# Optimization experiments

Hardware: AMD Instinct MI355X
Metric: run time of the kernel (lower is better)

The kernel has to match this reference:

```python
import jax, jax.numpy as jnp
import numpy as np

V, H, O = 256, 1024, 1024   # input_dim, hidden_dim, output_dim
B, T = 64, 512


def setup_inputs() -> dict:
    key = jax.random.key(0)
    ks = jax.random.split(key, 12)
    s = 1.0 / np.sqrt(H)  # torch nn.RNN / nn.Linear init range
    u = lambda k, shp: jax.random.uniform(k, shp, jnp.float32, -s, s)
    return {
        "x": jax.random.randint(ks[0], (B, T), 0, V),
        "W_ih_f": u(ks[1], (H, V)), "W_hh_f": u(ks[2], (H, H)),
        "b_ih_f": u(ks[3], (H,)),   "b_hh_f": u(ks[4], (H,)),
        "W_ih_b": u(ks[5], (H, V)), "W_hh_b": u(ks[6], (H, H)),
        "b_ih_b": u(ks[7], (H,)),   "b_hh_b": u(ks[8], (H,)),
        "W_fc": u(ks[9], (O, 2 * H)), "b_fc": u(ks[10], (O,)),
    }


def _scan_rnn(xW, W_hh):
    # xW: [T,B,H] precomputed input contribution (x W_ih^T + b_ih + b_hh)
    def step(h, xw):
        h = jnp.tanh(xw + h @ W_hh.T)
        return h, h
    h0 = jnp.zeros((xW.shape[1], W_hh.shape[0]), xW.dtype)
    _, hs = jax.lax.scan(step, h0, xW)
    return hs  # [T,B,H]


def reference(x, W_ih_f, W_hh_f, b_ih_f, b_hh_f,
              W_ih_b, W_hh_b, b_ih_b, b_hh_b, W_fc, b_fc):
    # one_hot(x, V) @ W_ih^T  ==  W_ih.T[x]  (gather; same math, no dense one-hot)
    xW_f = W_ih_f.T[x] + b_ih_f + b_hh_f          # [B,T,H]
    xW_b = W_ih_b.T[x] + b_ih_b + b_hh_b          # [B,T,H]
    hf = _scan_rnn(jnp.swapaxes(xW_f, 0, 1), W_hh_f)            # [T,B,H]
    hb = _scan_rnn(jnp.swapaxes(xW_b, 0, 1)[::-1], W_hh_b)[::-1]  # [T,B,H]
    out = jnp.swapaxes(jnp.concatenate([hf, hb], axis=-1), 0, 1)  # [B,T,2H]
    return out @ W_fc.T + b_fc                    # [B,T,O]
```

## Files before the change

### kernel.cpp

```cpp
#include <hip/hip_runtime.h>
#include <math.h>

#define B_ 64
#define T_ 512
#define H_ 1024
#define V_ 256
#define O_ 1024
#define KFC 2048

typedef short bf16x8 __attribute__((ext_vector_type(8)));
typedef _Float16 f16x8 __attribute__((ext_vector_type(8)));
typedef float f32x4 __attribute__((ext_vector_type(4)));
typedef int   i32x4 __attribute__((ext_vector_type(4)));
typedef unsigned long long u64x2 __attribute__((ext_vector_type(2)));

#define FLIP64 0x8000800080008000ULL

#define OFF_TABLE_F 0
#define OFF_TABLE_B 1048576
#define OFF_XT      2097152
#define OFF_WHH     2228224
#define OFF_WFC     6422528
#define OFF_HSF     10616832
#define OFF_HSB     77725696

__global__ void prep_kernel(const int* __restrict__ x,
    const float* __restrict__ WihF, const float* __restrict__ WhhF,
    const float* __restrict__ bihF, const float* __restrict__ bhhF,
    const float* __restrict__ WihB, const float* __restrict__ WhhB,
    const float* __restrict__ bihB, const float* __restrict__ bhhB,
    const float* __restrict__ Wfc,
    float* __restrict__ tableF, float* __restrict__ tableB,
    int* __restrict__ xT, short* __restrict__ whhpack,
    short* __restrict__ wfcpack, unsigned long long* __restrict__ hsz)
{
  const long NT1 = 524288, NT2 = 32768, NT3 = 2097152, NT4 = 2097152;
  const long NT5 = 16777216;
  const long total = NT1 + NT2 + NT3 + NT4 + NT5;
  for (long i = (long)blockIdx.x * blockDim.x + threadIdx.x; i < total;
       i += (long)gridDim.x * blockDim.x) {
    long j = i;
    if (j < NT1) {
      int d = (int)(j >> 18);
      int r = (int)(j & 262143);
      int v = r >> 10, h = r & 1023;
      const float* Wih = d ? WihB : WihF;
      const float* bi  = d ? bihB : bihF;
      const float* bh  = d ? bhhB : bhhF;
      (d ? tableB : tableF)[r] = Wih[h * V_ + v] + bi[h] + bh[h];
      continue;
    }
    j -= NT1;
    if (j < NT2) {
      int t = (int)(j >> 6), bb = (int)(j & 63);
      xT[j] = x[bb * T_ + t];
      continue;
    }
    j -= NT2;
    if (j < NT3) {
      int d = (int)(j >> 20);
      int r = (int)(j & 1048575);
      int jj = r & 7;
      int lanei = (r >> 3) & 63;
      int kt = (r >> 9) & 31;
      int cti = (r >> 14) & 3;
      int csi = (r >> 16) & 15;
      int c = csi * 64 + cti * 16 + (lanei & 15);
      int k = kt * 32 + (lanei >> 4) * 8 + jj;
      float w = (d ? WhhB : WhhF)[c * H_ + k];
      _Float16 wh = (_Float16)w;
      whhpack[j] = __builtin_bit_cast(short, wh);
      continue;
    }
    j -= NT3;
    if (j < NT4) {
      int jj = (int)(j & 7);
      int lanei = (int)((j >> 3) & 63);
      int nti = (int)((j >> 9) & 3);
      int k32 = (int)((j >> 11) & 63);
      int obi = (int)(j >> 17);
      int o = obi * 64 + nti * 16 + (lanei & 15);
      int k = k32 * 32 + (lanei >> 4) * 8 + jj;
      _Float16 wf = (_Float16)Wfc[(long)o * KFC + k];
      wfcpack[j] = __builtin_bit_cast(short, wf);
      continue;
    }
    j -= NT4;
    hsz[j] = 0ULL;
    continue;
  }
}

__global__ __launch_bounds__(256, 1)
void rnn_kernel(const int* __restrict__ xT,
                const float* __restrict__ tableF, const float* __restrict__ tableB,
                const short* __restrict__ whhpack,
                unsigned long long* __restrict__ hsfF,
                unsigned long long* __restrict__ hsfB)
{
  extern __shared__ char lds[];
  char* ldsW = lds;
  char* ldsH = lds + 131072;
  const int tid = threadIdx.x;
  const int wg = blockIdx.x;
  const int dir = wg >> 6;
  const int bt = (wg >> 4) & 3;
  const int cs = wg & 15;
  const int lane = tid & 63;
  const int ct = tid >> 6;
  const int row = bt * 16 + (lane & 15);
  const int c4 = cs * 64 + ct * 16 + (lane >> 4) * 4;
  const float* table = dir ? tableB : tableF;
  unsigned long long* hsx = dir ? hsfB : hsfF;
  const int pub_off = bt * 4096 + (c4 >> 5) * 128 + ((c4 >> 2) & 1) * 64 +
                      (lane & 15) + ((c4 >> 3) & 3) * 16;

  {
    const i32x4* wsrc = (const i32x4*)whhpack + (size_t)(dir * 16 + cs) * 8192;
    i32x4* wdst = (i32x4*)ldsW;
    #pragma unroll
    for (int it = 0; it < 32; ++it)
      wdst[it * 256 + tid] = wsrc[it * 256 + tid];
  }
  __syncthreads();

  const f32x4 zv = {0.f, 0.f, 0.f, 0.f};

  {
    int t0 = dir ? 511 : 0;
    int v = xT[t0 * 64 + row];
    f32x4 xwv = *(const f32x4*)(table + v * 1024 + c4);
    unsigned long long hx = 0;
    #pragma unroll
    for (int r = 0; r < 4; ++r) {
      float e = __expf(2.0f * xwv[r]);
      float h = (e - 1.0f) / (e + 1.0f);
      union { _Float16 f; unsigned short u; } cv; cv.f = (_Float16)h;
      unsigned short u = (cv.u == 0x8000u) ? 0u : cv.u;
      hx |= (unsigned long long)(u ^ 0x8000u) << (16 * r);
    }
    __hip_atomic_store(hsx + (size_t)t0 * 16384 + pub_off, hx,
                       __ATOMIC_RELAXED, __HIP_MEMORY_SCOPE_AGENT);
  }

  for (int s = 1; s < 512; ++s) {
    const int t = dir ? (511 - s) : s;
    const int tprev = dir ? (t + 1) : (t - 1);
    int v = xT[t * 64 + row];
    f32x4 xwv = *(const f32x4*)(table + v * 1024 + c4);

    const unsigned long long* sp =
        hsx + (size_t)tprev * 16384 + bt * 4096 + tid * 2;
    unsigned long long va[8], vb[8];
    for (;;) {
      int miss = 0;
      #pragma unroll
      for (int jj = 0; jj < 8; ++jj) {
        va[jj] = __hip_atomic_load(sp + jj * 512, __ATOMIC_RELAXED,
                                   __HIP_MEMORY_SCOPE_AGENT);
        vb[jj] = __hip_atomic_load(sp + jj * 512 + 1, __ATOMIC_RELAXED,
                                   __HIP_MEMORY_SCOPE_AGENT);
      }
      #pragma unroll
      for (int jj = 0; jj < 8; ++jj)
        miss |= (va[jj] == 0ULL) | (vb[jj] == 0ULL);
      if (!__ballot(miss)) break;
      __builtin_amdgcn_s_sleep(1);
    }
    #pragma unroll
    for (int jj = 0; jj < 8; ++jj) {
      u64x2 w; w[0] = va[jj] ^ FLIP64; w[1] = vb[jj] ^ FLIP64;
      *(u64x2*)(ldsH + jj * 4096 + tid * 16) = w;
    }
    __syncthreads();

    f32x4 acc4[4] = {zv, zv, zv, zv};
    #pragma unroll
    for (int kt = 0; kt < 32; ++kt) {
      f16x8 af = *(const f16x8*)(ldsW + ((ct * 32 + kt) * 64 + lane) * 16);
      u64x2 bv;
      bv[0] = *(const unsigned long long*)(ldsH + (kt * 128 + lane) * 8);
      bv[1] = *(const unsigned long long*)(ldsH + (kt * 128 + 64 + lane) * 8);
      f16x8 bf = __builtin_bit_cast(f16x8, bv);
      acc4[kt & 3] =
          __builtin_amdgcn_mfma_f32_16x16x32_f16(af, bf, acc4[kt & 3], 0, 0, 0);
    }
    __syncthreads();

    f32x4 accs = (acc4[0] + acc4[1]) + (acc4[2] + acc4[3]);
    unsigned long long hx = 0;
    #pragma unroll
    for (int r = 0; r < 4; ++r) {
      float zz = accs[r] + xwv[r];
      float e = __expf(2.0f * zz);
      float h = (e - 1.0f) / (e + 1.0f);
      union { _Float16 f; unsigned short u; } cv; cv.f = (_Float16)h;
      unsigned short u = (cv.u == 0x8000u) ? 0u : cv.u;
      hx |= (unsigned long long)(u ^ 0x8000u) << (16 * r);
    }
    __hip_atomic_store(hsx + (size_t)t * 16384 + pub_off, hx,
                       __ATOMIC_RELAXED, __HIP_MEMORY_SCOPE_AGENT);
  }
}

__global__ __launch_bounds__(256, 4)
void fc_kernel(const unsigned long long* __restrict__ hsfF,
               const unsigned long long* __restrict__ hsfB,
               const short* __restrict__ wfcpack, const float* __restrict__ bfc,
               float* __restrict__ out)
{
  __shared__ unsigned long long Alds[1024];
  __shared__ short Blds[4096];
  const int tid = threadIdx.x;
  const int lane = tid & 63;
  const int wv = tid >> 6;
  const int mt2 = wv & 1;
  const int nt2 = wv >> 1;
  const int t = blockIdx.x;
  const int ob = blockIdx.y;
  const int ik = tid >> 7;
  const int btl = (tid >> 5) & 3;
  const int w4 = (tid & 31) * 4;

  const i32x4 flip32 = {(int)0x80008000, (int)0x80008000,
                        (int)0x80008000, (int)0x80008000};
  f32x4 z = {0.f, 0.f, 0.f, 0.f};
  f32x4 acc[2][2] = {{z, z}, {z, z}};

  for (int kc = 0; kc < 32; ++kc) {
    {
      const unsigned long long* src =
          (kc < 16 ? hsfF : hsfB) + (size_t)t * 16384;
      int kt0 = (kc & 15) * 2;
      const unsigned long long* ap = src + btl * 4096 + (kt0 + ik) * 128 + w4;
      i32x4 a01 = *(const i32x4*)ap ^ flip32;
      i32x4 a23 = *(const i32x4*)(ap + 2) ^ flip32;
      *(i32x4*)&Alds[(btl * 2 + ik) * 128 + w4] = a01;
      *(i32x4*)&Alds[(btl * 2 + ik) * 128 + w4 + 2] = a23;
    }
    {
      const i32x4* src = (const i32x4*)(wfcpack + ((size_t)ob * 64 + kc * 2) * 2048);
      i32x4* dst = (i32x4*)Blds;
      dst[tid] = src[tid];
      dst[tid + 256] = src[tid + 256];
    }
    __syncthreads();
    #pragma unroll
    for (int k2 = 0; k2 < 2; ++k2) {
      f16x8 afr[2];
      #pragma unroll
      for (int mi = 0; mi < 2; ++mi) {
        int btm = mt2 * 2 + mi;
        u64x2 av;
        av[0] = Alds[(btm * 2 + k2) * 128 + lane];
        av[1] = Alds[(btm * 2 + k2) * 128 + 64 + lane];
        afr[mi] = __builtin_bit_cast(f16x8, av);
      }
      #pragma unroll
      for (int ni = 0; ni < 2; ++ni) {
        int ntg = nt2 * 2 + ni;
        f16x8 bfr = *(const f16x8*)((const char*)Blds + ((k2 * 4 + ntg) * 64 + lane) * 16);
        #pragma unroll
        for (int mi = 0; mi < 2; ++mi)
          acc[mi][ni] = __builtin_amdgcn_mfma_f32_16x16x32_f16(afr[mi], bfr, acc[mi][ni], 0, 0, 0);
      }
    }
    __syncthreads();
  }
  #pragma unroll
  for (int mi = 0; mi < 2; ++mi) {
    #pragma unroll
    for (int ni = 0; ni < 2; ++ni) {
      int o = ob * 64 + nt2 * 32 + ni * 16 + (lane & 15);
      float bias = bfc[o];
      #pragma unroll
      for (int r = 0; r < 4; ++r) {
        int b = mt2 * 32 + mi * 16 + (lane >> 4) * 4 + r;
        out[(size_t)(b * 512 + t) * O_ + o] = acc[mi][ni][r] + bias;
      }
    }
  }
}

extern "C" void kernel_launch(void* const* d_in, const int* in_sizes, int n_in,
                              void* d_out, int out_size, void* d_ws, size_t ws_size,
                              hipStream_t stream) {
  const int* x = (const int*)d_in[0];
  const float* WihF = (const float*)d_in[1];
  const float* WhhF = (const float*)d_in[2];
  const float* bihF = (const float*)d_in[3];
  const float* bhhF = (const float*)d_in[4];
  const float* WihB = (const float*)d_in[5];
  const float* WhhB = (const float*)d_in[6];
  const float* bihB = (const float*)d_in[7];
  const float* bhhB = (const float*)d_in[8];
  const float* Wfc  = (const float*)d_in[9];
  const float* bfc  = (const float*)d_in[10];
  float* out = (float*)d_out;
  char* ws = (char*)d_ws;

  float* tableF = (float*)(ws + OFF_TABLE_F);
  float* tableB = (float*)(ws + OFF_TABLE_B);
  int* xT = (int*)(ws + OFF_XT);
  short* whhpack = (short*)(ws + OFF_WHH);
  short* wfcpack = (short*)(ws + OFF_WFC);
  unsigned long long* hsfF = (unsigned long long*)(ws + OFF_HSF);
  unsigned long long* hsfB = (unsigned long long*)(ws + OFF_HSB);

  hipFuncSetAttribute((const void*)rnn_kernel,
                      hipFuncAttributeMaxDynamicSharedMemorySize, 163840);

  prep_kernel<<<dim3(2048), dim3(256), 0, stream>>>(
      x, WihF, WhhF, bihF, bhhF, WihB, WhhB, bihB, bhhB, Wfc,
      tableF, tableB, xT, whhpack, wfcpack, hsfF);
  rnn_kernel<<<dim3(128), dim3(256), 163840, stream>>>(
      xT, tableF, tableB, whhpack, hsfF, hsfB);
  fc_kernel<<<dim3(512, 16), dim3(256), 0, stream>>>(
      hsfF, hsfB, wfcpack, bfc, out);
}
```

Measured before the change: 1.583 ms.

## Feed recurrent MFMAs directly from global hidden state with pipelined polling

Each wave now loads its own B-operand fragments of the previous hidden state straight from global memory into registers, in four K-groups. It polls each group for readiness and overlaps issuing the next group's loads with MFMAs on the current group. This removes the LDS staging buffer and both per-step __syncthreads barriers, so the dynamic LDS request drops. The cost is that every wave issues its own redundant global loads and spin-waits, which adds memory traffic and register pressure.

```diff
diff --git a/kernel.cpp b/kernel.cpp
--- a/kernel.cpp
+++ b/kernel.cpp
@@ -100,7 +100,6 @@
 {
   extern __shared__ char lds[];
   char* ldsW = lds;
-  char* ldsH = lds + 131072;
   const int tid = threadIdx.x;
   const int wg = blockIdx.x;
   const int dir = wg >> 6;
@@ -150,42 +149,61 @@
     f32x4 xwv = *(const f32x4*)(table + v * 1024 + c4);
 
     const unsigned long long* sp =
-        hsx + (size_t)tprev * 16384 + bt * 4096 + tid * 2;
-    unsigned long long va[8], vb[8];
-    for (;;) {
-      int miss = 0;
-      #pragma unroll
-      for (int jj = 0; jj < 8; ++jj) {
-        va[jj] = __hip_atomic_load(sp + jj * 512, __ATOMIC_RELAXED,
-                                   __HIP_MEMORY_SCOPE_AGENT);
-        vb[jj] = __hip_atomic_load(sp + jj * 512 + 1, __ATOMIC_RELAXED,
-                                   __HIP_MEMORY_SCOPE_AGENT);
-      }
-      #pragma unroll
-      for (int jj = 0; jj < 8; ++jj)
-        miss |= (va[jj] == 0ULL) | (vb[jj] == 0ULL);
-      if (!__ballot(miss)) break;
-      __builtin_amdgcn_s_sleep(1);
-    }
-    #pragma unroll
-    for (int jj = 0; jj < 8; ++jj) {
-      u64x2 w; w[0] = va[jj] ^ FLIP64; w[1] = vb[jj] ^ FLIP64;
-      *(u64x2*)(ldsH + jj * 4096 + tid * 16) = w;
-    }
-    __syncthreads();
+        hsx + (size_t)tprev * 16384 + bt * 4096 + lane;
 
     f32x4 acc4[4] = {zv, zv, zv, zv};
-    #pragma unroll
-    for (int kt = 0; kt < 32; ++kt) {
-      f16x8 af = *(const f16x8*)(ldsW + ((ct * 32 + kt) * 64 + lane) * 16);
-      u64x2 bv;
-      bv[0] = *(const unsigned long long*)(ldsH + (kt * 128 + lane) * 8);
-      bv[1] = *(const unsigned long long*)(ldsH + (kt * 128 + 64 + lane) * 8);
-      f16x8 bf = __builtin_bit_cast(f16x8, bv);
-      acc4[kt & 3] =
-          __builtin_amdgcn_mfma_f32_16x16x32_f16(af, bf, acc4[kt & 3], 0, 0, 0);
-    }
-    __syncthreads();
+    unsigned long long A0[8], B0[8], A1[8], B1[8];
+
+#define ISSUEG(g, A, B) do { \
+    _Pragma("unroll") \
+    for (int i = 0; i < 8; ++i) { \
+      (A)[i] = __hip_atomic_load(sp + ((g) * 8 + i) * 128, \
+                                 __ATOMIC_RELAXED, __HIP_MEMORY_SCOPE_AGENT); \
+      (B)[i] = __hip_atomic_load(sp + ((g) * 8 + i) * 128 + 64, \
+                                 __ATOMIC_RELAXED, __HIP_MEMORY_SCOPE_AGENT); \
+    } \
+  } while (0)
+
+#define POLLG(g, A, B) do { \
+    for (;;) { \
+      int miss = 0; \
+      _Pragma("unroll") \
+      for (int i = 0; i < 8; ++i) \
+        miss |= ((A)[i] == 0ULL) | ((B)[i] == 0ULL); \
+      if (!__ballot(miss)) break; \
+      __builtin_amdgcn_s_sleep(1); \
+      ISSUEG(g, A, B); \
+    } \
+  } while (0)
+
+#define MFMAG(g, A, B) do { \
+    _Pragma("unroll") \
+    for (int i = 0; i < 8; ++i) { \
+      int kt = (g) * 8 + i; \
+      f16x8 af = *(const f16x8*)(ldsW + ((ct * 32 + kt) * 64 + lane) * 16); \
+      u64x2 bv; bv[0] = (A)[i] ^ FLIP64; bv[1] = (B)[i] ^ FLIP64; \
+      f16x8 bf = __builtin_bit_cast(f16x8, bv); \
+      acc4[i & 3] = \
+          __builtin_amdgcn_mfma_f32_16x16x32_f16(af, bf, acc4[i & 3], 0, 0, 0); \
+    } \
+  } while (0)
+
+    ISSUEG(0, A0, B0);
+    ISSUEG(1, A1, B1);
+    POLLG(0, A0, B0);
+    MFMAG(0, A0, B0);
+    ISSUEG(2, A0, B0);
+    POLLG(1, A1, B1);
+    MFMAG(1, A1, B1);
+    ISSUEG(3, A1, B1);
+    POLLG(2, A0, B0);
+    MFMAG(2, A0, B0);
+    POLLG(3, A1, B1);
+    MFMAG(3, A1, B1);
+
+#undef ISSUEG
+#undef POLLG
+#undef MFMAG
 
     f32x4 accs = (acc4[0] + acc4[1]) + (acc4[2] + acc4[3]);
     unsigned long long hx = 0;
@@ -308,12 +326,12 @@
   unsigned long long* hsfB = (unsigned long long*)(ws + OFF_HSB);
 
   hipFuncSetAttribute((const void*)rnn_kernel,
-                      hipFuncAttributeMaxDynamicSharedMemorySize, 163840);
+                      hipFuncAttributeMaxDynamicSharedMemorySize, 131072);
 
   prep_kernel<<<dim3(2048), dim3(256), 0, stream>>>(
       x, WihF, WhhF, bihF, bhhF, WihB, WhhB, bihB, bhhB, Wfc,
       tableF, tableB, xT, whhpack, wfcpack, hsfF);
-  rnn_kernel<<<dim3(128), dim3(256), 163840, stream>>>(
+  rnn_kernel<<<dim3(128), dim3(256), 131072, stream>>>(
       xT, tableF, tableB, whhpack, hsfF, hsfB);
   fc_kernel<<<dim3(512, 16), dim3(256), 0, stream>>>(
       hsfF, hsfB, wfcpack, bfc, out);
```

Result: slower. 2.292 ms (+44.8%).

## Split hidden-state polling into halves and overlap second half with first-half MFMAs

Applied to the files above, without the earlier changes.

The recurrent step now loads the previous hidden state in two halves. It polls only the first half, then starts the first 16 MFMA k-tiles while the second half is still arriving, and only then waits on and stages the second half. The trailing __syncthreads is dropped and the LDS barriers are replaced with explicit lgkmcnt waits plus s_barrier. The tanh now uses a fast reciprocal instead of a division. The aim is to hide inter-block latency on the critical serial path, at the cost of relying on barrier ordering to avoid LDS write-after-read hazards across steps and some precision loss in tanh.

```diff
diff --git a/kernel.cpp b/kernel.cpp
--- a/kernel.cpp
+++ b/kernel.cpp
@@ -23,6 +23,11 @@
 #define OFF_WFC     6422528
 #define OFF_HSF     10616832
 #define OFF_HSB     77725696
+
+__device__ __forceinline__ float fast_tanh(float zz) {
+  float e = __expf(2.0f * zz);
+  return 1.0f - 2.0f * __builtin_amdgcn_rcpf(e + 1.0f);
+}
 
 __global__ void prep_kernel(const int* __restrict__ x,
     const float* __restrict__ WihF, const float* __restrict__ WhhF,
@@ -133,8 +138,7 @@
     unsigned long long hx = 0;
     #pragma unroll
     for (int r = 0; r < 4; ++r) {
-      float e = __expf(2.0f * xwv[r]);
-      float h = (e - 1.0f) / (e + 1.0f);
+      float h = fast_tanh(xwv[r]);
       union { _Float16 f; unsigned short u; } cv; cv.f = (_Float16)h;
       unsigned short u = (cv.u == 0x8000u) ? 0u : cv.u;
       hx |= (unsigned long long)(u ^ 0x8000u) << (16 * r);
@@ -142,6 +146,8 @@
     __hip_atomic_store(hsx + (size_t)t0 * 16384 + pub_off, hx,
                        __ATOMIC_RELAXED, __HIP_MEMORY_SCOPE_AGENT);
   }
+
+#define LDX(p) __hip_atomic_load((p), __ATOMIC_RELAXED, __HIP_MEMORY_SCOPE_AGENT)
 
   for (int s = 1; s < 512; ++s) {
     const int t = dir ? (511 - s) : s;
@@ -151,32 +157,43 @@
 
     const unsigned long long* sp =
         hsx + (size_t)tprev * 16384 + bt * 4096 + tid * 2;
-    unsigned long long va[8], vb[8];
+    unsigned long long a0[4], b0[4], a1[4], b1[4];
+    #pragma unroll
+    for (int i = 0; i < 4; ++i) {
+      a0[i] = LDX(sp + i * 512);
+      b0[i] = LDX(sp + i * 512 + 1);
+    }
+    #pragma unroll
+    for (int i = 0; i < 4; ++i) {
+      a1[i] = LDX(sp + (4 + i) * 512);
+      b1[i] = LDX(sp + (4 + i) * 512 + 1);
+    }
+
     for (;;) {
       int miss = 0;
       #pragma unroll
-      for (int jj = 0; jj < 8; ++jj) {
-        va[jj] = __hip_atomic_load(sp + jj * 512, __ATOMIC_RELAXED,
-                                   __HIP_MEMORY_SCOPE_AGENT);
-        vb[jj] = __hip_atomic_load(sp + jj * 512 + 1, __ATOMIC_RELAXED,
-                                   __HIP_MEMORY_SCOPE_AGENT);
-      }
-      #pragma unroll
-      for (int jj = 0; jj < 8; ++jj)
-        miss |= (va[jj] == 0ULL) | (vb[jj] == 0ULL);
+      for (int i = 0; i < 4; ++i)
+        miss |= (a0[i] == 0ULL) | (b0[i] == 0ULL);
       if (!__ballot(miss)) break;
       __builtin_amdgcn_s_sleep(1);
-    }
-    #pragma unroll
-    for (int jj = 0; jj < 8; ++jj) {
-      u64x2 w; w[0] = va[jj] ^ FLIP64; w[1] = vb[jj] ^ FLIP64;
+      #pragma unroll
+      for (int i = 0; i < 4; ++i) {
+        a0[i] = LDX(sp + i * 512);
+        b0[i] = LDX(sp + i * 512 + 1);
+      }
+    }
+    #pragma unroll
+    for (int jj = 0; jj < 4; ++jj) {
+      u64x2 w; w[0] = a0[jj] ^ FLIP64; w[1] = b0[jj] ^ FLIP64;
       *(u64x2*)(ldsH + jj * 4096 + tid * 16) = w;
     }
-    __syncthreads();
+    asm volatile("s_waitcnt lgkmcnt(0)" ::: "memory");
+    __builtin_amdgcn_s_barrier();
+    asm volatile("" ::: "memory");
 
     f32x4 acc4[4] = {zv, zv, zv, zv};
     #pragma unroll
-    for (int kt = 0; kt < 32; ++kt) {
+    for (int kt = 0; kt < 16; ++kt) {
       f16x8 af = *(const f16x8*)(ldsW + ((ct * 32 + kt) * 64 + lane) * 16);
       u64x2 bv;
       bv[0] = *(const unsigned long long*)(ldsH + (kt * 128 + lane) * 8);
@@ -185,15 +202,45 @@
       acc4[kt & 3] =
           __builtin_amdgcn_mfma_f32_16x16x32_f16(af, bf, acc4[kt & 3], 0, 0, 0);
     }
-    __syncthreads();
+
+    for (;;) {
+      int miss = 0;
+      #pragma unroll
+      for (int i = 0; i < 4; ++i)
+        miss |= (a1[i] == 0ULL) | (b1[i] == 0ULL);
+      if (!__ballot(miss)) break;
+      __builtin_amdgcn_s_sleep(1);
+      #pragma unroll
+      for (int i = 0; i < 4; ++i) {
+        a1[i] = LDX(sp + (4 + i) * 512);
+        b1[i] = LDX(sp + (4 + i) * 512 + 1);
+      }
+    }
+    #pragma unroll
+    for (int jj = 0; jj < 4; ++jj) {
+      u64x2 w; w[0] = a1[jj] ^ FLIP64; w[1] = b1[jj] ^ FLIP64;
+      *(u64x2*)(ldsH + (4 + jj) * 4096 + tid * 16) = w;
+    }
+    asm volatile("s_waitcnt lgkmcnt(0)" ::: "memory");
+    __builtin_amdgcn_s_barrier();
+    asm volatile("" ::: "memory");
+
+    #pragma unroll
+    for (int kt = 16; kt < 32; ++kt) {
+      f16x8 af = *(const f16x8*)(ldsW + ((ct * 32 + kt) * 64 + lane) * 16);
+      u64x2 bv;
+      bv[0] = *(const unsigned long long*)(ldsH + (kt * 128 + lane) * 8);
+      bv[1] = *(const unsigned long long*)(ldsH + (kt * 128 + 64 + lane) * 8);
+      f16x8 bf = __builtin_bit_cast(f16x8, bv);
+      acc4[kt & 3] =
+          __builtin_amdgcn_mfma_f32_16x16x32_f16(af, bf, acc4[kt & 3], 0, 0, 0);
+    }
 
     f32x4 accs = (acc4[0] + acc4[1]) + (acc4[2] + acc4[3]);
     unsigned long long hx = 0;
     #pragma unroll
     for (int r = 0; r < 4; ++r) {
-      float zz = accs[r] + xwv[r];
-      float e = __expf(2.0f * zz);
-      float h = (e - 1.0f) / (e + 1.0f);
+      float h = fast_tanh(accs[r] + xwv[r]);
       union { _Float16 f; unsigned short u; } cv; cv.f = (_Float16)h;
       unsigned short u = (cv.u == 0x8000u) ? 0u : cv.u;
       hx |= (unsigned long long)(u ^ 0x8000u) << (16 * r);
@@ -201,6 +248,7 @@
     __hip_atomic_store(hsx + (size_t)t * 16384 + pub_off, hx,
                        __ATOMIC_RELAXED, __HIP_MEMORY_SCOPE_AGENT);
   }
+#undef LDX
 }
 
 __global__ __launch_bounds__(256, 4)
```

Measured after the change: 1.642 ms. 1.04x slower.
